# Performance work log

Measured on AMD Instinct MI355X. Metric: run time of the kernel, lower is better.

Reference implementation:

```python
import jax, jax.numpy as jnp
import numpy as np

EMBEDDING_DIM = 128
CODEBOOK_SIZE = 8192
COMMITMENT_COST = 0.25


def setup_inputs() -> dict:
    key = jax.random.key(0)
    k1, k2 = jax.random.split(key)
    inputs = jax.random.normal(k1, (8, 2048, EMBEDDING_DIM), dtype=jnp.float32)
    embeddings = jax.random.normal(k2, (EMBEDDING_DIM, CODEBOOK_SIZE), dtype=jnp.float32)
    return {"inputs": inputs, "embeddings": embeddings}


def reference(inputs, embeddings):
    # inputs: [B, T, D]; embeddings: [D, K]
    B, T, D = inputs.shape
    K = embeddings.shape[1]
    flat = inputs.reshape(-1, D)                      # [N, D]
    sim = flat @ embeddings                           # [N, K]
    dists = (jnp.sum(flat * flat, axis=1, keepdims=True)
             - 2.0 * sim
             + jnp.sum(embeddings * embeddings, axis=0, keepdims=True))
    idx_flat = jnp.argmax(-dists, axis=1)             # [N], matches tf.argmax(-d)
    encodings = jax.nn.one_hot(idx_flat, K, dtype=inputs.dtype)  # [N, K]
    encoding_indices = idx_flat.reshape(B, T)
    quantized = jnp.take(embeddings.T, encoding_indices, axis=0)  # [B, T, D]
    e_latent_loss = jnp.mean((jax.lax.stop_gradient(quantized) - inputs) ** 2)
    q_latent_loss = jnp.mean((quantized - jax.lax.stop_gradient(inputs)) ** 2)
    loss = q_latent_loss + COMMITMENT_COST * e_latent_loss
    quantized = inputs + jax.lax.stop_gradient(quantized - inputs)  # straight-through
    return quantized, encodings, encoding_indices, loss
```

## Files before the change

kernel.cpp:

```cpp
#include <hip/hip_runtime.h>

#define D 128
#define K 8192
#define N 16384
#define BM 32
#define BN 128
#define NCH (K / BN)
#define GRP 4
#define THREADS 256
#define CAND_CAP 1024
#define DELTA 0.5f
#define RMIN_INIT 0xFF800000u

typedef __attribute__((ext_vector_type(4))) float f32x4;
typedef __attribute__((ext_vector_type(16))) float f32x16;
typedef __attribute__((ext_vector_type(8))) short short8;

__device__ __forceinline__ unsigned short f2bf(float f) {
    unsigned int b = __float_as_uint(f);
    return (unsigned short)((b + 0x7FFFu + ((b >> 16) & 1u)) >> 16);
}
__device__ __forceinline__ unsigned int fsort(float f) {
    unsigned int b = __float_as_uint(f);
    return b ^ ((unsigned int)((int)b >> 31) | 0x80000000u);
}
__device__ __forceinline__ float funsort(unsigned int u) {
    return __uint_as_float((u & 0x80000000u) ? (u ^ 0x80000000u) : ~u);
}

__device__ __forceinline__ void lds_barrier() {
    asm volatile("s_waitcnt lgkmcnt(0)" ::: "memory");
    __builtin_amdgcn_s_barrier();
}

__global__ __launch_bounds__(256) void prep_kernel(const float* __restrict__ E,
        unsigned short* __restrict__ e1t, unsigned short* __restrict__ augt,
        float* __restrict__ e2t, float* __restrict__ enorm) {
    __shared__ float esum[8][32];
    const int t = threadIdx.x;
    const int kl = t & 31, dg = t >> 5;
    const int k = blockIdx.x * 32 + kl;
    float s = 0.f;
    __align__(16) unsigned short tmpb[16];
    __align__(16) float tmpf[16];
#pragma unroll
    for (int j = 0; j < 16; ++j) {
        float v = E[(size_t)(dg * 16 + j) * K + k];
        s += v * v;
        tmpb[j] = f2bf(v);
        tmpf[j] = v;
    }
    *(f32x4*)(e1t + (size_t)k * D + dg * 16) = *(const f32x4*)tmpb;
    *(f32x4*)(e1t + (size_t)k * D + dg * 16 + 8) = *(const f32x4*)(tmpb + 8);
    if (e2t) {
#pragma unroll
        for (int q = 0; q < 4; ++q)
            *(f32x4*)(e2t + (size_t)k * D + dg * 16 + 4 * q) = *(const f32x4*)(tmpf + 4 * q);
    }
    esum[dg][kl] = s;
    __syncthreads();
    if (t < 32) {
        float e = 0.f;
#pragma unroll
        for (int g = 0; g < 8; ++g) e += esum[g][t];
        const int kk = blockIdx.x * 32 + t;
        enorm[kk] = e;
        unsigned short hi = f2bf(e);
        float hif = __uint_as_float((unsigned int)hi << 16);
        unsigned short lo = f2bf(e - hif);
        __align__(16) unsigned short av[8] = {hi, lo, 0, 0, 0, 0, 0, 0};
        *(f32x4*)(augt + (size_t)kk * 8) = *(const f32x4*)av;
    }
}

template<int E2T>
__global__ __launch_bounds__(THREADS, 2) void main_kernel(
        const float* __restrict__ X, const float* __restrict__ E,
        const unsigned short* __restrict__ e1t, const unsigned short* __restrict__ augt,
        const float* __restrict__ e2t, const float* __restrict__ enorm,
        float* __restrict__ out, float* __restrict__ partials) {
    __shared__ __align__(16) unsigned short b_s[2][BN * D];
    __shared__ __align__(16) unsigned short aug_s[2][BN * 8];
    __shared__ unsigned long long cand[CAND_CAP];
    __shared__ unsigned long long best[BM];
    __shared__ unsigned int rmin[BM];
    __shared__ int candn;

    const int t = threadIdx.x;
    const int wid = t >> 6, l = t & 63;
    const int l31 = l & 31, lh = l >> 5;
    const int wn = wid;
    const int rowbase = blockIdx.x * BM;

    float* qout = out;
    float* enc = out + (size_t)N * D;
    float* idxout = enc + (size_t)N * K;

    if (t < BM) { rmin[t] = RMIN_INIT; best[t] = ~0ull; }
    if (t == 0) candn = 0;

    short8 afr[8];
    {
        const int row = rowbase + l31;
#pragma unroll
        for (int ks = 0; ks < 8; ++ks) {
            const float* xp = X + (size_t)row * D + ks * 16 + lh * 8;
            f32x4 v0 = *(const f32x4*)xp;
            f32x4 v1 = *(const f32x4*)(xp + 4);
            short8 a;
            a[0] = (short)f2bf(-2.f * v0[0]); a[1] = (short)f2bf(-2.f * v0[1]);
            a[2] = (short)f2bf(-2.f * v0[2]); a[3] = (short)f2bf(-2.f * v0[3]);
            a[4] = (short)f2bf(-2.f * v1[0]); a[5] = (short)f2bf(-2.f * v1[1]);
            a[6] = (short)f2bf(-2.f * v1[2]); a[7] = (short)f2bf(-2.f * v1[3]);
            afr[ks] = a;
        }
    }
    short8 a_aug;
    {
        const short one = (short)0x3F80;
        a_aug[0] = (lh == 0) ? one : (short)0;
        a_aug[1] = (lh == 0) ? one : (short)0;
        a_aug[2] = 0; a_aug[3] = 0; a_aug[4] = 0;
        a_aug[5] = 0; a_aug[6] = 0; a_aug[7] = 0;
    }

    f32x4 sreg[8];
    f32x4 avreg;
    {
        const f32x4* gs = (const f32x4*)e1t;
#pragma unroll
        for (int i = 0; i < 8; ++i) sreg[i] = gs[t + THREADS * i];
        if (t < 128) avreg = *(const f32x4*)(augt + (size_t)t * 8);
#pragma unroll
        for (int i = 0; i < 8; ++i) {
            int unit = t + THREADS * i;
            int c = unit >> 4, slot = unit & 15;
            *(f32x4*)((char*)&b_s[0][0] + c * 256 + ((slot ^ (c & 15)) << 4)) = sreg[i];
        }
        if (t < 128) *(f32x4*)((char*)&aug_s[0][0] + t * 16) = avreg;
    }

    int cur = 0;
    for (int cg = 0; cg < NCH / GRP; ++cg) {
        float dsave[GRP][16];
#pragma unroll
        for (int g = 0; g < GRP; ++g) {
            const int ch = cg * GRP + g;
            if (ch + 1 < NCH) {
                const f32x4* gs = (const f32x4*)(e1t + (size_t)(ch + 1) * BN * D);
#pragma unroll
                for (int i = 0; i < 8; ++i) sreg[i] = gs[t + THREADS * i];
                if (t < 128) avreg = *(const f32x4*)(augt + (size_t)(ch + 1) * BN * 8 + t * 8);
            }
            lds_barrier();

            {
                const f32x4 z = {0.f, 0.f, 0.f, 0.f};
#pragma unroll
                for (int i = 0; i < 4; ++i) {
                    int unit = t + THREADS * i;
                    int row = unit >> 5, cu = unit & 31;
                    __builtin_nontemporal_store(z,
                        (f32x4*)(enc + (size_t)(rowbase + row) * K + ch * BN + cu * 4));
                }
            }

            f32x16 acc;
#pragma unroll
            for (int r = 0; r < 16; ++r) acc[r] = 0.f;
#pragma unroll
            for (int ks = 0; ks < 8; ++ks) {
                const int c = wn * 32 + l31;
                const int slot = ks * 2 + lh;
                short8 bf = *(const short8*)((const char*)&b_s[cur][0] + c * 256 +
                                             ((slot ^ (c & 15)) << 4));
                acc = __builtin_amdgcn_mfma_f32_32x32x16_bf16(afr[ks], bf, acc, 0, 0, 0);
            }
            {
                const int c = wn * 32 + l31;
                short8 ba = {0, 0, 0, 0, 0, 0, 0, 0};
                if (lh == 0) ba = *(const short8*)((const char*)&aug_s[cur][0] + c * 16);
                acc = __builtin_amdgcn_mfma_f32_32x32x16_bf16(a_aug, ba, acc, 0, 0, 0);
            }
#pragma unroll
            for (int r = 0; r < 16; ++r) dsave[g][r] = acc[r];

            if (ch + 1 < NCH) {
#pragma unroll
                for (int i = 0; i < 8; ++i) {
                    int unit = t + THREADS * i;
                    int c = unit >> 4, slot = unit & 15;
                    *(f32x4*)((char*)&b_s[cur ^ 1][0] + c * 256 + ((slot ^ (c & 15)) << 4)) = sreg[i];
                }
                if (t < 128) *(f32x4*)((char*)&aug_s[cur ^ 1][0] + t * 16) = avreg;
            }
            cur ^= 1;
        }

        float lmin[16];
#pragma unroll
        for (int r = 0; r < 16; ++r)
            lmin[r] = fminf(fminf(dsave[0][r], dsave[1][r]),
                            fminf(dsave[2][r], dsave[3][r]));
#pragma unroll
        for (int m = 1; m <= 16; m <<= 1)
#pragma unroll
            for (int r = 0; r < 16; ++r)
                lmin[r] = fminf(lmin[r], __shfl_xor(lmin[r], m, 64));

        float thrv[16];
#pragma unroll
        for (int q = 0; q < 4; ++q) {
            const int base = 8 * q + 4 * lh;
            uint4 rv = *(const uint4*)&rmin[base];
            thrv[4 * q + 0] = funsort(rv.x);
            thrv[4 * q + 1] = funsort(rv.y);
            thrv[4 * q + 2] = funsort(rv.z);
            thrv[4 * q + 3] = funsort(rv.w);
        }

#pragma unroll
        for (int r = 0; r < 16; ++r) {
            const int ro = (r & 3) + 8 * (r >> 2) + 4 * lh;
            const float te = fminf(thrv[r], lmin[r]) + DELTA;
#pragma unroll
            for (int g = 0; g < GRP; ++g) {
                if (dsave[g][r] < te) {
                    const int col = (cg * GRP + g) * BN + wn * 32 + l31;
                    int ci = atomicAdd(&candn, 1);
                    if (ci < CAND_CAP)
                        cand[ci] = ((unsigned long long)fsort(dsave[g][r]) << 32) |
                                   ((unsigned long long)ro << 13) | (unsigned)col;
                }
            }
            if (l31 == 0 && lmin[r] < thrv[r])
                atomicMin(&rmin[ro], fsort(lmin[r]));
        }
    }

    __syncthreads();

    {
        int n = candn; if (n > CAND_CAP) n = CAND_CAP;
        for (int i = wid; i < n; i += 4) {
            const unsigned long long e = cand[i];
            const float dta = funsort((unsigned int)(e >> 32));
            const int ro = (int)((e >> 13) & 63u);
            const int col = (int)(e & 8191u);
            if (dta < funsort(rmin[ro]) + DELTA) {
                const int row = rowbase + ro;
                float x0 = X[(size_t)row * D + l];
                float x1 = X[(size_t)row * D + 64 + l];
                float e0, e1;
                if (E2T) {
                    e0 = e2t[(size_t)col * D + l];
                    e1 = e2t[(size_t)col * D + 64 + l];
                } else {
                    e0 = E[(size_t)l * K + col];
                    e1 = E[(size_t)(l + 64) * K + col];
                }
                float s = x0 * e0 + x1 * e1;
#pragma unroll
                for (int m = 1; m <= 32; m <<= 1) s += __shfl_xor(s, m, 64);
                if (l == 0) {
                    float dtx = enorm[col] - 2.f * s;
                    atomicMin(&best[ro],
                        ((unsigned long long)fsort(dtx) << 32) | (unsigned)col);
                }
            }
        }
    }
    __syncthreads();

    float* red = (float*)&b_s[0][0];
    if (t < BM) {
        const int k = (int)(best[t] & 8191ull);
        idxout[rowbase + t] = (float)k;
        __builtin_nontemporal_store(1.0f, &enc[(size_t)(rowbase + t) * K + k]);
    }

    const int rr = t >> 3, sL = t & 7;
    const int row = rowbase + rr;
    const int kb = (int)(best[rr] & 8191ull);
    float part = 0.f;
#pragma unroll
    for (int j = 0; j < 4; ++j) {
        const int d0 = sL * 16 + 4 * j;
        f32x4 xv = *(const f32x4*)(X + (size_t)row * D + d0);
        f32x4 ev;
        if (E2T) {
            ev = *(const f32x4*)(e2t + (size_t)kb * D + d0);
        } else {
#pragma unroll
            for (int u = 0; u < 4; ++u) ev[u] = E[(size_t)(d0 + u) * K + kb];
        }
        f32x4 qv;
#pragma unroll
        for (int u = 0; u < 4; ++u) {
            float df = ev[u] - xv[u];
            qv[u] = xv[u] + df;
            part += df * df;
        }
        *(f32x4*)(qout + (size_t)row * D + d0) = qv;
    }
    red[t] = part;
    __syncthreads();
#pragma unroll
    for (int off = THREADS / 2; off > 0; off >>= 1) {
        if (t < off) red[t] += red[t + off];
        __syncthreads();
    }
    if (t == 0) partials[blockIdx.x] = red[0];
}

__global__ __launch_bounds__(256) void loss_kernel(const float* __restrict__ partials,
                                                   float* __restrict__ out) {
    __shared__ float red[256];
    const int t = threadIdx.x;
    red[t] = partials[t] + partials[t + 256];
    __syncthreads();
    for (int off = 128; off > 0; off >>= 1) {
        if (t < off) red[t] += red[t + off];
        __syncthreads();
    }
    if (t == 0) {
        float mean = red[0] / (float)((size_t)N * D);
        out[(size_t)N * D + (size_t)N * K + N] = mean + 0.25f * mean;
    }
}

extern "C" void kernel_launch(void* const* d_in, const int* in_sizes, int n_in,
                              void* d_out, int out_size, void* d_ws, size_t ws_size,
                              hipStream_t stream) {
    const float* X = (const float*)d_in[0];
    const float* E = (const float*)d_in[1];
    float* out = (float*)d_out;
    char* ws = (char*)d_ws;

    const size_t E1T_B = (size_t)K * D * 2;
    const size_t AUG_B = (size_t)K * 8 * 2;
    const size_t E2T_B = (size_t)K * D * 4;
    const bool use_e2t = ws_size >= E1T_B + AUG_B + E2T_B + 64 * 1024;

    unsigned short* e1t = (unsigned short*)ws;
    unsigned short* augt = (unsigned short*)(ws + E1T_B);
    float* e2t; float* enorm; float* partials;
    if (use_e2t) {
        e2t = (float*)(ws + E1T_B + AUG_B);
        enorm = (float*)(ws + E1T_B + AUG_B + E2T_B);
        partials = enorm + K;
    } else {
        e2t = nullptr;
        enorm = (float*)(ws + E1T_B + AUG_B);
        partials = enorm + K;
    }

    hipLaunchKernelGGL(prep_kernel, dim3(K / 32), dim3(256), 0, stream,
                       E, e1t, augt, e2t, enorm);
    if (use_e2t)
        hipLaunchKernelGGL((main_kernel<1>), dim3(N / BM), dim3(THREADS), 0, stream,
                           X, E, e1t, augt, e2t, enorm, out, partials);
    else
        hipLaunchKernelGGL((main_kernel<0>), dim3(N / BM), dim3(THREADS), 0, stream,
                           X, E, e1t, augt, e2t, enorm, out, partials);
    hipLaunchKernelGGL(loss_kernel, dim3(1), dim3(256), 0, stream, partials, out);
}
```

Before: 173.1 us.

## Specialize warps into compute, loader, and zero-store roles

Splits the four waves of each block by role. Waves 0-1 each compute two 32-column MFMA tiles per chunk and do the candidate filtering. Wave 2 alone loads the next codebook chunk into the other LDS buffer, and wave 3 alone streams zero stores into the one-hot encoding stripe. The aim is to overlap global loads and the large zero-fill traffic with MFMA work instead of having every wave serialize all three. The cost is that fewer waves issue MFMAs, and a single wave must carry the whole load and the whole store bandwidth, which could make it the bottleneck.

```diff
diff --git a/kernel.cpp b/kernel.cpp
--- a/kernel.cpp
+++ b/kernel.cpp
@@ -89,18 +89,19 @@
     const int t = threadIdx.x;
     const int wid = t >> 6, l = t & 63;
     const int l31 = l & 31, lh = l >> 5;
-    const int wn = wid;
     const int rowbase = blockIdx.x * BM;
 
     float* qout = out;
     float* enc = out + (size_t)N * D;
     float* idxout = enc + (size_t)N * K;
+    float* stripe = enc + (size_t)rowbase * K;
 
     if (t < BM) { rmin[t] = RMIN_INIT; best[t] = ~0ull; }
     if (t == 0) candn = 0;
 
     short8 afr[8];
-    {
+    short8 a_aug;
+    if (wid < 2) {
         const int row = rowbase + l31;
 #pragma unroll
         for (int ks = 0; ks < 8; ++ks) {
@@ -114,9 +115,6 @@
             a[6] = (short)f2bf(-2.f * v1[2]); a[7] = (short)f2bf(-2.f * v1[3]);
             afr[ks] = a;
         }
-    }
-    short8 a_aug;
-    {
         const short one = (short)0x3F80;
         a_aug[0] = (lh == 0) ? one : (short)0;
         a_aug[1] = (lh == 0) ? one : (short)0;
@@ -124,117 +122,133 @@
         a_aug[5] = 0; a_aug[6] = 0; a_aug[7] = 0;
     }
 
-    f32x4 sreg[8];
-    f32x4 avreg;
-    {
-        const f32x4* gs = (const f32x4*)e1t;
-#pragma unroll
-        for (int i = 0; i < 8; ++i) sreg[i] = gs[t + THREADS * i];
-        if (t < 128) avreg = *(const f32x4*)(augt + (size_t)t * 8);
-#pragma unroll
-        for (int i = 0; i < 8; ++i) {
-            int unit = t + THREADS * i;
-            int c = unit >> 4, slot = unit & 15;
-            *(f32x4*)((char*)&b_s[0][0] + c * 256 + ((slot ^ (c & 15)) << 4)) = sreg[i];
-        }
-        if (t < 128) *(f32x4*)((char*)&aug_s[0][0] + t * 16) = avreg;
-    }
-
+    if (wid == 2) {
+#pragma unroll
+        for (int b = 0; b < 4; ++b) {
+            f32x4 v[8];
+#pragma unroll
+            for (int j = 0; j < 8; ++j)
+                v[j] = ((const f32x4*)e1t)[l + 64 * (b * 8 + j)];
+#pragma unroll
+            for (int j = 0; j < 8; ++j) {
+                int unit = l + 64 * (b * 8 + j);
+                int c = unit >> 4, slot = unit & 15;
+                *(f32x4*)((char*)&b_s[0][0] + c * 256 + ((slot ^ (c & 15)) << 4)) = v[j];
+            }
+        }
+        f32x4 a0 = ((const f32x4*)augt)[l];
+        f32x4 a1 = ((const f32x4*)augt)[l + 64];
+        *(f32x4*)((char*)&aug_s[0][0] + l * 16) = a0;
+        *(f32x4*)((char*)&aug_s[0][0] + (l + 64) * 16) = a1;
+    }
+
+    const f32x4 z = {0.f, 0.f, 0.f, 0.f};
     int cur = 0;
     for (int cg = 0; cg < NCH / GRP; ++cg) {
-        float dsave[GRP][16];
+        f32x16 dsv[GRP][2];
 #pragma unroll
         for (int g = 0; g < GRP; ++g) {
             const int ch = cg * GRP + g;
-            if (ch + 1 < NCH) {
-                const f32x4* gs = (const f32x4*)(e1t + (size_t)(ch + 1) * BN * D);
-#pragma unroll
-                for (int i = 0; i < 8; ++i) sreg[i] = gs[t + THREADS * i];
-                if (t < 128) avreg = *(const f32x4*)(augt + (size_t)(ch + 1) * BN * 8 + t * 8);
-            }
             lds_barrier();
 
-            {
-                const f32x4 z = {0.f, 0.f, 0.f, 0.f};
-#pragma unroll
-                for (int i = 0; i < 4; ++i) {
-                    int unit = t + THREADS * i;
-                    int row = unit >> 5, cu = unit & 31;
-                    __builtin_nontemporal_store(z,
-                        (f32x4*)(enc + (size_t)(rowbase + row) * K + ch * BN + cu * 4));
+            if (wid < 2) {
+#pragma unroll
+                for (int sp = 0; sp < 2; ++sp) {
+                    const int c = (wid * 2 + sp) * 32 + l31;
+                    f32x16 acc;
+#pragma unroll
+                    for (int r = 0; r < 16; ++r) acc[r] = 0.f;
+#pragma unroll
+                    for (int ks = 0; ks < 8; ++ks) {
+                        const int slot = ks * 2 + lh;
+                        short8 bf = *(const short8*)((const char*)&b_s[cur][0] + c * 256 +
+                                                     ((slot ^ (c & 15)) << 4));
+                        acc = __builtin_amdgcn_mfma_f32_32x32x16_bf16(afr[ks], bf, acc, 0, 0, 0);
+                    }
+                    short8 ba = {0, 0, 0, 0, 0, 0, 0, 0};
+                    if (lh == 0) ba = *(const short8*)((const char*)&aug_s[cur][0] + c * 16);
+                    acc = __builtin_amdgcn_mfma_f32_32x32x16_bf16(a_aug, ba, acc, 0, 0, 0);
+#pragma unroll
+                    for (int r = 0; r < 16; ++r) dsv[g][sp][r] = acc[r];
                 }
-            }
-
-            f32x16 acc;
-#pragma unroll
-            for (int r = 0; r < 16; ++r) acc[r] = 0.f;
-#pragma unroll
-            for (int ks = 0; ks < 8; ++ks) {
-                const int c = wn * 32 + l31;
-                const int slot = ks * 2 + lh;
-                short8 bf = *(const short8*)((const char*)&b_s[cur][0] + c * 256 +
-                                             ((slot ^ (c & 15)) << 4));
-                acc = __builtin_amdgcn_mfma_f32_32x32x16_bf16(afr[ks], bf, acc, 0, 0, 0);
-            }
-            {
-                const int c = wn * 32 + l31;
-                short8 ba = {0, 0, 0, 0, 0, 0, 0, 0};
-                if (lh == 0) ba = *(const short8*)((const char*)&aug_s[cur][0] + c * 16);
-                acc = __builtin_amdgcn_mfma_f32_32x32x16_bf16(a_aug, ba, acc, 0, 0, 0);
-            }
-#pragma unroll
-            for (int r = 0; r < 16; ++r) dsave[g][r] = acc[r];
-
-            if (ch + 1 < NCH) {
-#pragma unroll
-                for (int i = 0; i < 8; ++i) {
-                    int unit = t + THREADS * i;
-                    int c = unit >> 4, slot = unit & 15;
-                    *(f32x4*)((char*)&b_s[cur ^ 1][0] + c * 256 + ((slot ^ (c & 15)) << 4)) = sreg[i];
+            } else if (wid == 2) {
+                if (ch + 1 < NCH) {
+                    const f32x4* gs = (const f32x4*)(e1t + (size_t)(ch + 1) * BN * D);
+#pragma unroll
+                    for (int b = 0; b < 4; ++b) {
+                        f32x4 v[8];
+#pragma unroll
+                        for (int j = 0; j < 8; ++j)
+                            v[j] = gs[l + 64 * (b * 8 + j)];
+#pragma unroll
+                        for (int j = 0; j < 8; ++j) {
+                            int unit = l + 64 * (b * 8 + j);
+                            int c = unit >> 4, slot = unit & 15;
+                            *(f32x4*)((char*)&b_s[cur ^ 1][0] + c * 256 +
+                                      ((slot ^ (c & 15)) << 4)) = v[j];
+                        }
+                    }
+                    const f32x4* ga = (const f32x4*)(augt + (size_t)(ch + 1) * BN * 8);
+                    f32x4 a0 = ga[l];
+                    f32x4 a1 = ga[l + 64];
+                    *(f32x4*)((char*)&aug_s[cur ^ 1][0] + l * 16) = a0;
+                    *(f32x4*)((char*)&aug_s[cur ^ 1][0] + (l + 64) * 16) = a1;
                 }
-                if (t < 128) *(f32x4*)((char*)&aug_s[cur ^ 1][0] + t * 16) = avreg;
+            } else {
+                float* base = stripe + (size_t)ch * 4096;
+#pragma unroll
+                for (int j = 0; j < 16; ++j)
+                    __builtin_nontemporal_store(z, (f32x4*)(base + j * 256 + l * 4));
             }
             cur ^= 1;
         }
 
-        float lmin[16];
-#pragma unroll
-        for (int r = 0; r < 16; ++r)
-            lmin[r] = fminf(fminf(dsave[0][r], dsave[1][r]),
-                            fminf(dsave[2][r], dsave[3][r]));
-#pragma unroll
-        for (int m = 1; m <= 16; m <<= 1)
-#pragma unroll
-            for (int r = 0; r < 16; ++r)
-                lmin[r] = fminf(lmin[r], __shfl_xor(lmin[r], m, 64));
-
-        float thrv[16];
-#pragma unroll
-        for (int q = 0; q < 4; ++q) {
-            const int base = 8 * q + 4 * lh;
-            uint4 rv = *(const uint4*)&rmin[base];
-            thrv[4 * q + 0] = funsort(rv.x);
-            thrv[4 * q + 1] = funsort(rv.y);
-            thrv[4 * q + 2] = funsort(rv.z);
-            thrv[4 * q + 3] = funsort(rv.w);
-        }
-
-#pragma unroll
-        for (int r = 0; r < 16; ++r) {
-            const int ro = (r & 3) + 8 * (r >> 2) + 4 * lh;
-            const float te = fminf(thrv[r], lmin[r]) + DELTA;
-#pragma unroll
-            for (int g = 0; g < GRP; ++g) {
-                if (dsave[g][r] < te) {
-                    const int col = (cg * GRP + g) * BN + wn * 32 + l31;
-                    int ci = atomicAdd(&candn, 1);
-                    if (ci < CAND_CAP)
-                        cand[ci] = ((unsigned long long)fsort(dsave[g][r]) << 32) |
-                                   ((unsigned long long)ro << 13) | (unsigned)col;
-                }
-            }
-            if (l31 == 0 && lmin[r] < thrv[r])
-                atomicMin(&rmin[ro], fsort(lmin[r]));
+        if (wid < 2) {
+            float lmin[16];
+#pragma unroll
+            for (int r = 0; r < 16; ++r) {
+                float m0 = fminf(dsv[0][0][r], dsv[0][1][r]);
+                float m1 = fminf(dsv[1][0][r], dsv[1][1][r]);
+                float m2 = fminf(dsv[2][0][r], dsv[2][1][r]);
+                float m3 = fminf(dsv[3][0][r], dsv[3][1][r]);
+                lmin[r] = fminf(fminf(m0, m1), fminf(m2, m3));
+            }
+#pragma unroll
+            for (int m = 1; m <= 16; m <<= 1)
+#pragma unroll
+                for (int r = 0; r < 16; ++r)
+                    lmin[r] = fminf(lmin[r], __shfl_xor(lmin[r], m, 64));
+
+            float thrv[16];
+#pragma unroll
+            for (int q = 0; q < 4; ++q) {
+                const int base = 8 * q + 4 * lh;
+                uint4 rv = *(const uint4*)&rmin[base];
+                thrv[4 * q + 0] = funsort(rv.x);
+                thrv[4 * q + 1] = funsort(rv.y);
+                thrv[4 * q + 2] = funsort(rv.z);
+                thrv[4 * q + 3] = funsort(rv.w);
+            }
+
+#pragma unroll
+            for (int r = 0; r < 16; ++r) {
+                const int ro = (r & 3) + 8 * (r >> 2) + 4 * lh;
+                const float te = fminf(thrv[r], lmin[r]) + DELTA;
+#pragma unroll
+                for (int g = 0; g < GRP; ++g)
+#pragma unroll
+                    for (int sp = 0; sp < 2; ++sp) {
+                        if (dsv[g][sp][r] < te) {
+                            const int col = (cg * GRP + g) * BN + (wid * 2 + sp) * 32 + l31;
+                            int ci = atomicAdd(&candn, 1);
+                            if (ci < CAND_CAP)
+                                cand[ci] = ((unsigned long long)fsort(dsv[g][sp][r]) << 32) |
+                                           ((unsigned long long)ro << 13) | (unsigned)col;
+                        }
+                    }
+                if (l31 == 0 && lmin[r] < thrv[r])
+                    atomicMin(&rmin[ro], fsort(lmin[r]));
+            }
         }
     }
 
```

Result: slower. 653.3 us (+277.3%).
